# Optimization experiments

Hardware: AMD Instinct MI355X
Metric: run time of the kernel (lower is better)

The kernel has to match this reference:

```python
import jax, jax.numpy as jnp
import numpy as np

N_NODES = 100000
N_EDGES = 1600000
IN_FEATS = 128
N_HIDDEN = 128
N_CLASSES = 47


def setup_inputs() -> dict:
    key = jax.random.key(0)
    ks = jax.random.split(key, 9)
    x = jax.random.normal(ks[0], (N_NODES, IN_FEATS), dtype=jnp.float32)
    src = jax.random.randint(ks[1], (N_EDGES,), 0, N_NODES, dtype=jnp.int32)
    dst = jax.random.randint(ks[2], (N_EDGES,), 0, N_NODES, dtype=jnp.int32)
    s = 0.05
    return {
        "x": x, "src": src, "dst": dst,
        "Ws0": jax.random.normal(ks[3], (IN_FEATS, N_HIDDEN), jnp.float32) * s,
        "Wn0": jax.random.normal(ks[4], (IN_FEATS, N_HIDDEN), jnp.float32) * s,
        "b0": jnp.zeros((N_HIDDEN,), jnp.float32),
        "Ws1": jax.random.normal(ks[5], (N_HIDDEN, N_HIDDEN), jnp.float32) * s,
        "Wn1": jax.random.normal(ks[6], (N_HIDDEN, N_HIDDEN), jnp.float32) * s,
        "b1": jnp.zeros((N_HIDDEN,), jnp.float32),
        "Ws2": jax.random.normal(ks[7], (N_HIDDEN, N_CLASSES), jnp.float32) * s,
        "Wn2": jax.random.normal(ks[8], (N_HIDDEN, N_CLASSES), jnp.float32) * s,
        "b2": jnp.zeros((N_CLASSES,), jnp.float32),
    }


def _sage_layer(h, src, dst, inv_deg, Ws, Wn, b):
    # weighted (w=1) mean aggregation over in-neighbors: sum(h[src]) / in_degree
    msg = h[src]  # [E, d] irregular gather
    neigh = jax.ops.segment_sum(msg, dst, num_segments=N_NODES) * inv_deg[:, None]
    # DGL SAGEConv 'mean': fc_self(h_self) + fc_neigh(h_neigh), bias on self branch
    return h @ Ws + neigh @ Wn + b


def reference(x, src, dst, Ws0, Wn0, b0, Ws1, Wn1, b1, Ws2, Wn2, b2):
    deg = jax.ops.segment_sum(jnp.ones_like(dst, dtype=x.dtype), dst, num_segments=N_NODES)
    inv_deg = 1.0 / jnp.maximum(deg, 1.0)
    h = _sage_layer(x, src, dst, inv_deg, Ws0, Wn0, b0)
    h = jax.nn.relu(h)  # dropout is identity (eval / p=0)
    h = _sage_layer(h, src, dst, inv_deg, Ws1, Wn1, b1)
    h = jax.nn.relu(h)
    h = _sage_layer(h, src, dst, inv_deg, Ws2, Wn2, b2)
    return jax.nn.log_softmax(h, axis=-1)
```

## Files before the change

### kernel.cpp

```cpp
#include <hip/hip_runtime.h>
#include <hip/hip_bf16.h>

#define NN 100000
#define NE 1600000
#define F 128
#define NCLS 47

#define NPB 256
#define BUCKETS 391
#define ABLK 512
#define ACHUNK (NE / ABLK)

typedef __attribute__((ext_vector_type(8))) short short8;
typedef __attribute__((ext_vector_type(8))) unsigned short u16x8;
typedef __attribute__((ext_vector_type(4))) float f32x4;

#define MFMA16(A, B, C) __builtin_amdgcn_mfma_f32_16x16x32_bf16(A, B, C, 0, 0, 0)

__device__ __forceinline__ unsigned short b16(float f) {
    unsigned int u = __builtin_bit_cast(unsigned int, f);
    unsigned int r = u + 0x7FFFu + ((u >> 16) & 1u);
    return (unsigned short)(r >> 16);
}
__device__ __forceinline__ float bflo(unsigned int u) { return __builtin_bit_cast(float, u << 16); }
__device__ __forceinline__ float bfhi(unsigned int u) { return __builtin_bit_cast(float, u & 0xFFFF0000u); }

__global__ void __launch_bounds__(256) k_bhist(const int* __restrict__ dst,
                                               int* __restrict__ bucket_cnt) {
    __shared__ int hist[BUCKETS];
    const int t = threadIdx.x;
    for (int i = t; i < BUCKETS; i += 256) hist[i] = 0;
    __syncthreads();
    const int e0 = blockIdx.x * ACHUNK;
    for (int i = t; i < ACHUNK; i += 256) atomicAdd(&hist[dst[e0 + i] >> 8], 1);
    __syncthreads();
    for (int i = t; i < BUCKETS; i += 256)
        if (hist[i]) atomicAdd(&bucket_cnt[i], hist[i]);
}

__global__ void k_bscan(const int* __restrict__ bucket_cnt, int* __restrict__ bucket_off,
                        int* __restrict__ cursor) {
    const int lane = threadIdx.x & 63;
    int run = 0;
#pragma unroll
    for (int c = 0; c < 7; c++) {
        int idx = c * 64 + lane;
        int v = (idx < BUCKETS) ? bucket_cnt[idx] : 0;
        int s = v;
#pragma unroll
        for (int off = 1; off < 64; off <<= 1) {
            int n = __shfl_up(s, off);
            if (lane >= off) s += n;
        }
        int excl = run + s - v;
        if (idx <= BUCKETS) {
            bucket_off[idx] = excl;
            cursor[idx] = excl;
        }
        run += __shfl(s, 63);
    }
}

__global__ void __launch_bounds__(256) k_bscatter(const int* __restrict__ src,
                                                  const int* __restrict__ dst,
                                                  int* __restrict__ cursor,
                                                  unsigned int* __restrict__ ebuf) {
    __shared__ int hist[BUCKETS];
    __shared__ int base[BUCKETS];
    __shared__ int rank[BUCKETS];
    const int t = threadIdx.x;
    for (int i = t; i < BUCKETS; i += 256) {
        hist[i] = 0;
        rank[i] = 0;
    }
    __syncthreads();
    const int e0 = blockIdx.x * ACHUNK;
    for (int i = t; i < ACHUNK; i += 256) atomicAdd(&hist[dst[e0 + i] >> 8], 1);
    __syncthreads();
    for (int i = t; i < BUCKETS; i += 256) {
        int h = hist[i];
        base[i] = h ? atomicAdd(&cursor[i], h) : 0;
    }
    __syncthreads();
    for (int i = t; i < ACHUNK; i += 256) {
        unsigned int s = (unsigned int)src[e0 + i];
        int d = dst[e0 + i];
        int b = d >> 8;
        int r = atomicAdd(&rank[b], 1);
        ebuf[base[b] + r] = s | ((unsigned int)(d & 255) << 24);
    }
}

__global__ void __launch_bounds__(256) k_bcsr(const unsigned int* __restrict__ ebuf,
                                              const int* __restrict__ bucket_off,
                                              int* __restrict__ row_off,
                                              float* __restrict__ inv_deg,
                                              int* __restrict__ col) {
    __shared__ int cnt[NPB];
    __shared__ int ro[NPB];
    __shared__ int wsum[4];
    const int t = threadIdx.x, lane = t & 63, wid = t >> 6;
    cnt[t] = 0;
    __syncthreads();
    const int e0 = bucket_off[blockIdx.x], e1 = bucket_off[blockIdx.x + 1];
    for (int i = e0 + t; i < e1; i += 256) atomicAdd(&cnt[ebuf[i] >> 24], 1);
    __syncthreads();
    int v = cnt[t];
    int run = v;
#pragma unroll
    for (int off = 1; off < 64; off <<= 1) {
        int n = __shfl_up(run, off);
        if (lane >= off) run += n;
    }
    if (lane == 63) wsum[wid] = run;
    __syncthreads();
    int woff = e0;
#pragma unroll
    for (int wv = 0; wv < 4; wv++)
        if (wv < wid) woff += wsum[wv];
    int excl = woff + run - v;
    int node = (blockIdx.x << 8) + t;
    if (node < NN) {
        row_off[node] = excl;
        inv_deg[node] = 1.0f / fmaxf((float)v, 1.0f);
    }
    if (blockIdx.x == BUCKETS - 1 && t == 0) row_off[NN] = NE;
    ro[t] = excl;
    cnt[t] = 0;
    __syncthreads();
    for (int i = e0 + t; i < e1; i += 256) {
        unsigned int e = ebuf[i];
        int d = e >> 24;
        int p = atomicAdd(&cnt[d], 1);
        col[ro[d] + p] = (int)(e & 0xFFFFFFu);
    }
}

__global__ void k_cvt(const float* __restrict__ x, unsigned short* __restrict__ xb,
                      unsigned short* __restrict__ h1b, unsigned short* __restrict__ hw2b) {
    int t = blockIdx.x * blockDim.x + threadIdx.x;
    if (blockIdx.x == 0) {
        int tt = threadIdx.x;
        if (tt < 128) {
            xb[(size_t)NN * F + tt] = 0;
            h1b[(size_t)NN * F + tt] = 0;
            if (tt < 64) hw2b[(size_t)NN * 64 + tt] = 0;
        }
    }
    if (t >= NN * F / 8) return;
    const float4* x4 = (const float4*)x;
    float4 a = x4[t * 2], b = x4[t * 2 + 1];
    u16x8 o;
    o[0] = b16(a.x); o[1] = b16(a.y); o[2] = b16(a.z); o[3] = b16(a.w);
    o[4] = b16(b.x); o[5] = b16(b.y); o[6] = b16(b.z); o[7] = b16(b.w);
    ((u16x8*)xb)[t] = o;
}

__global__ void k_pack_all(const float* __restrict__ Ws0, const float* __restrict__ Wn0,
                           const float* __restrict__ Ws1, const float* __restrict__ Wn1,
                           const float* __restrict__ Ws2, const float* __restrict__ Wn2,
                           unsigned short* __restrict__ wp) {
    int idx = blockIdx.x * blockDim.x + threadIdx.x;
    if (idx >= 77824) return;
    const float* W;
    int base, ncols;
    if (idx < 65536) {
        int m = idx >> 14;
        W = (m == 0) ? Ws0 : (m == 1) ? Wn0 : (m == 2) ? Ws1 : Wn1;
        base = m << 14;
        ncols = 128;
    } else {
        int m = (idx - 65536) / 6144;
        W = m ? Wn2 : Ws2;
        base = 65536 + m * 6144;
        ncols = NCLS;
    }
    int li = idx - base;
    int nt = li >> 11;
    int r = li & 2047;
    int kk = r >> 9;
    int r2 = r & 511;
    int lane = r2 >> 3;
    int j = r2 & 7;
    int k = kk * 32 + ((lane >> 4) << 3) + j;
    int n = nt * 16 + (lane & 15);
    float v = (n < ncols) ? W[k * ncols + n] : 0.f;
    wp[idx] = b16(v);
}

__global__ void __launch_bounds__(256) k_aggb(const uint4* __restrict__ h4,
                                              const int* __restrict__ row_off,
                                              const int* __restrict__ col,
                                              const float* __restrict__ inv_deg,
                                              uint4* __restrict__ a4) {
    int node = (blockIdx.x * blockDim.x + threadIdx.x) >> 6;
    int lane = threadIdx.x & 63;
    if (node >= NN) return;
    int b = row_off[node], e = row_off[node + 1];
    int deg = e - b;
    const int g = lane >> 4, fl = lane & 15;
    float acc[8];
#pragma unroll
    for (int i = 0; i < 8; i++) acc[i] = 0.f;
    for (int base = 0; base < deg; base += 64) {
        int cnt = deg - base;
        if (cnt > 64) cnt = 64;
        int myc = col[b + base + (lane < cnt ? lane : 0)];
        for (int jj = 0; jj < cnt; jj += 16) {
            uint4 u[4];
#pragma unroll
            for (int k2 = 0; k2 < 4; k2++) {
                int r = jj + k2 * 4 + g;
                int c = __shfl(myc, r);
                c = (r < cnt) ? c : NN;
                u[k2] = h4[(size_t)(unsigned)c * 16u + fl];
            }
#pragma unroll
            for (int k2 = 0; k2 < 4; k2++) {
                uint4 v = u[k2];
                acc[0] += bflo(v.x); acc[1] += bfhi(v.x);
                acc[2] += bflo(v.y); acc[3] += bfhi(v.y);
                acc[4] += bflo(v.z); acc[5] += bfhi(v.z);
                acc[6] += bflo(v.w); acc[7] += bfhi(v.w);
            }
        }
    }
#pragma unroll
    for (int i = 0; i < 8; i++) {
        acc[i] += __shfl_xor(acc[i], 16);
        acc[i] += __shfl_xor(acc[i], 32);
    }
    if (g == 0) {
        float s = inv_deg[node];
        uint4 o;
        o.x = (unsigned)b16(acc[0] * s) | ((unsigned)b16(acc[1] * s) << 16);
        o.y = (unsigned)b16(acc[2] * s) | ((unsigned)b16(acc[3] * s) << 16);
        o.z = (unsigned)b16(acc[4] * s) | ((unsigned)b16(acc[5] * s) << 16);
        o.w = (unsigned)b16(acc[6] * s) | ((unsigned)b16(acc[7] * s) << 16);
        a4[(size_t)node * 16 + fl] = o;
    }
}

__global__ void __launch_bounds__(256) k_agg48(const uint4* __restrict__ hw4,
                                               const int* __restrict__ row_off,
                                               const int* __restrict__ col,
                                               const float* __restrict__ inv_deg,
                                               uint4* __restrict__ aggh4) {
    int node = (blockIdx.x * blockDim.x + threadIdx.x) >> 6;
    int lane = threadIdx.x & 63;
    if (node >= NN) return;
    int b = row_off[node], e = row_off[node + 1];
    int deg = e - b;
    const int g = lane >> 3, fl = lane & 7;
    float acc[8];
#pragma unroll
    for (int i = 0; i < 8; i++) acc[i] = 0.f;
    for (int base = 0; base < deg; base += 64) {
        int cnt = deg - base;
        if (cnt > 64) cnt = 64;
        int myc = col[b + base + (lane < cnt ? lane : 0)];
        for (int jj = 0; jj < cnt; jj += 16) {
            uint4 u[2];
#pragma unroll
            for (int k2 = 0; k2 < 2; k2++) {
                int r = jj + k2 * 8 + g;
                int c = __shfl(myc, r);
                c = (r < cnt) ? c : NN;
                u[k2] = hw4[(size_t)(unsigned)c * 8u + fl];
            }
#pragma unroll
            for (int k2 = 0; k2 < 2; k2++) {
                uint4 v = u[k2];
                acc[0] += bflo(v.x); acc[1] += bfhi(v.x);
                acc[2] += bflo(v.y); acc[3] += bfhi(v.y);
                acc[4] += bflo(v.z); acc[5] += bfhi(v.z);
                acc[6] += bflo(v.w); acc[7] += bfhi(v.w);
            }
        }
    }
#pragma unroll
    for (int i = 0; i < 8; i++) {
        acc[i] += __shfl_xor(acc[i], 8);
        acc[i] += __shfl_xor(acc[i], 16);
        acc[i] += __shfl_xor(acc[i], 32);
    }
    if (lane < 8) {
        float s = inv_deg[node];
        uint4 o;
        o.x = (unsigned)b16(acc[0] * s) | ((unsigned)b16(acc[1] * s) << 16);
        o.y = (unsigned)b16(acc[2] * s) | ((unsigned)b16(acc[3] * s) << 16);
        o.z = (unsigned)b16(acc[4] * s) | ((unsigned)b16(acc[5] * s) << 16);
        o.w = (unsigned)b16(acc[6] * s) | ((unsigned)b16(acc[7] * s) << 16);
        aggh4[(size_t)node * 8 + fl] = o;
    }
}

template <bool RELU>
__global__ void __launch_bounds__(256) k_layer(const unsigned short* __restrict__ hb,
                                               const unsigned short* __restrict__ ab,
                                               const unsigned short* __restrict__ wps,
                                               const unsigned short* __restrict__ wpn,
                                               const float* __restrict__ bias,
                                               unsigned short* __restrict__ outb) {
    const int wid = threadIdx.x >> 6, lane = threadIdx.x & 63;
    const int tile0 = blockIdx.x * 64;
    const short8* ws8 = (const short8*)wps;
    const short8* wn8 = (const short8*)wpn;
    short8 wf[2][2][4];
#pragma unroll
    for (int t = 0; t < 2; t++) {
        int nt = 2 * wid + t;
#pragma unroll
        for (int kk = 0; kk < 4; kk++) {
            wf[0][t][kk] = ws8[(nt * 4 + kk) * 64 + lane];
            wf[1][t][kk] = wn8[(nt * 4 + kk) * 64 + lane];
        }
    }
    const int rb = lane & 15, kq = lane >> 4;
    float bv[2];
#pragma unroll
    for (int t = 0; t < 2; t++) bv[t] = bias[(2 * wid + t) * 16 + rb];
    const short8* h8 = (const short8*)hb;
    const short8* a8 = (const short8*)ab;
    f32x4 zero = {0.f, 0.f, 0.f, 0.f};
    f32x4 acc[4][2];
#pragma unroll
    for (int m = 0; m < 4; m++)
#pragma unroll
        for (int t = 0; t < 2; t++) acc[m][t] = zero;
#pragma unroll
    for (int kk = 0; kk < 4; kk++) {
#pragma unroll
        for (int m = 0; m < 4; m++) {
            int row = tile0 + m * 16 + rb;
            int rc = row < NN ? row : NN - 1;
            int idx = rc * 16 + kk * 4 + kq;
            short8 af = h8[idx];
            short8 gf = a8[idx];
            acc[m][0] = MFMA16(af, wf[0][0][kk], acc[m][0]);
            acc[m][1] = MFMA16(af, wf[0][1][kk], acc[m][1]);
            acc[m][0] = MFMA16(gf, wf[1][0][kk], acc[m][0]);
            acc[m][1] = MFMA16(gf, wf[1][1][kk], acc[m][1]);
        }
    }
#pragma unroll
    for (int m = 0; m < 4; m++) {
#pragma unroll
        for (int reg = 0; reg < 4; reg++) {
            int row = tile0 + m * 16 + kq * 4 + reg;
            if (row < NN) {
#pragma unroll
                for (int t = 0; t < 2; t++) {
                    float v = acc[m][t][reg] + bv[t];
                    if (RELU) v = fmaxf(v, 0.f);
                    outb[(size_t)row * F + (2 * wid + t) * 16 + rb] = b16(v);
                }
            }
        }
    }
}

__global__ void __launch_bounds__(512) k_nmul(const unsigned short* __restrict__ hb,
                                              const unsigned short* __restrict__ wpn,
                                              unsigned short* __restrict__ hw) {
    const int wid = threadIdx.x >> 6, lane = threadIdx.x & 63;
    const int R0 = blockIdx.x * 128 + wid * 16;
    const short8* wn8 = (const short8*)wpn;
    short8 wf[3][4];
#pragma unroll
    for (int nt = 0; nt < 3; nt++)
#pragma unroll
        for (int kk = 0; kk < 4; kk++) wf[nt][kk] = wn8[(nt * 4 + kk) * 64 + lane];
    const int rb = lane & 15, kq = lane >> 4;
    const short8* h8 = (const short8*)hb;
    f32x4 zero = {0.f, 0.f, 0.f, 0.f};
    f32x4 acc[3] = {zero, zero, zero};
    int rowr = R0 + rb;
    int rc = rowr < NN ? rowr : NN - 1;
#pragma unroll
    for (int kk = 0; kk < 4; kk++) {
        short8 af = h8[rc * 16 + kk * 4 + kq];
#pragma unroll
        for (int nt = 0; nt < 3; nt++) acc[nt] = MFMA16(af, wf[nt][kk], acc[nt]);
    }
#pragma unroll
    for (int reg = 0; reg < 4; reg++) {
        int row = R0 + kq * 4 + reg;
        if (row < NN) {
#pragma unroll
            for (int nt = 0; nt < 3; nt++)
                hw[(size_t)row * 64 + nt * 16 + rb] = b16(acc[nt][reg]);
        }
    }
}

__global__ void __launch_bounds__(512) k_out2(const unsigned short* __restrict__ hb,
                                              const unsigned short* __restrict__ aggh,
                                              const unsigned short* __restrict__ wps,
                                              const float* __restrict__ bias,
                                              float* __restrict__ out) {
    const int wid = threadIdx.x >> 6, lane = threadIdx.x & 63;
    const int R0 = blockIdx.x * 128 + wid * 16;
    const short8* ws8 = (const short8*)wps;
    short8 wf[3][4];
#pragma unroll
    for (int nt = 0; nt < 3; nt++)
#pragma unroll
        for (int kk = 0; kk < 4; kk++) wf[nt][kk] = ws8[(nt * 4 + kk) * 64 + lane];
    const int rb = lane & 15, kq = lane >> 4;
    float bv[3];
    bool valid[3];
#pragma unroll
    for (int nt = 0; nt < 3; nt++) {
        int c = nt * 16 + rb;
        valid[nt] = c < NCLS;
        bv[nt] = valid[nt] ? bias[c] : 0.f;
    }
    const short8* h8 = (const short8*)hb;
    f32x4 zero = {0.f, 0.f, 0.f, 0.f};
    f32x4 acc[3] = {zero, zero, zero};
    int rowr = R0 + rb;
    int rc = rowr < NN ? rowr : NN - 1;
#pragma unroll
    for (int kk = 0; kk < 4; kk++) {
        short8 af = h8[rc * 16 + kk * 4 + kq];
#pragma unroll
        for (int nt = 0; nt < 3; nt++) acc[nt] = MFMA16(af, wf[nt][kk], acc[nt]);
    }
#pragma unroll
    for (int reg = 0; reg < 4; reg++) {
        int row = R0 + kq * 4 + reg;
        int rc2 = row < NN ? row : NN - 1;
        float v[3];
        float mx = -1e30f;
#pragma unroll
        for (int nt = 0; nt < 3; nt++) {
            float av = __builtin_bit_cast(
                float, (unsigned)aggh[(size_t)rc2 * 64 + nt * 16 + rb] << 16);
            v[nt] = acc[nt][reg] + av + bv[nt];
            if (valid[nt]) mx = fmaxf(mx, v[nt]);
        }
        for (int off = 1; off < 16; off <<= 1) mx = fmaxf(mx, __shfl_xor(mx, off));
        float s = 0.f;
#pragma unroll
        for (int nt = 0; nt < 3; nt++)
            if (valid[nt]) s += expf(v[nt] - mx);
        for (int off = 1; off < 16; off <<= 1) s += __shfl_xor(s, off);
        float L = mx + logf(s);
        if (row < NN) {
#pragma unroll
            for (int nt = 0; nt < 3; nt++)
                if (valid[nt]) out[(size_t)row * NCLS + nt * 16 + rb] = v[nt] - L;
        }
    }
}

extern "C" void kernel_launch(void* const* d_in, const int* in_sizes, int n_in,
                              void* d_out, int out_size, void* d_ws, size_t ws_size,
                              hipStream_t stream) {
    (void)in_sizes; (void)n_in; (void)out_size; (void)ws_size;
    const float* x = (const float*)d_in[0];
    const int* src = (const int*)d_in[1];
    const int* dst = (const int*)d_in[2];
    const float* Ws0 = (const float*)d_in[3];
    const float* Wn0 = (const float*)d_in[4];
    const float* b0 = (const float*)d_in[5];
    const float* Ws1 = (const float*)d_in[6];
    const float* Wn1 = (const float*)d_in[7];
    const float* b1 = (const float*)d_in[8];
    const float* Ws2 = (const float*)d_in[9];
    const float* Wn2 = (const float*)d_in[10];
    const float* b2 = (const float*)d_in[11];
    float* out = (float*)d_out;

    char* w = (char*)d_ws;
    size_t off = 0;
    auto alloc = [&](size_t bytes) -> char* {
        char* p = w + off;
        off = (off + bytes + 255) & ~(size_t)255;
        return p;
    };
    int* row_off = (int*)alloc((size_t)(NN + 1) * 4);
    int* col = (int*)alloc((size_t)NE * 4);
    float* inv_deg = (float*)alloc((size_t)NN * 4);
    int* bucket_cnt = (int*)alloc((size_t)(BUCKETS + 1) * 4);
    int* bucket_off = (int*)alloc((size_t)(BUCKETS + 1) * 4);
    int* bcursor = (int*)alloc((size_t)(BUCKETS + 1) * 4);
    unsigned int* ebuf = (unsigned int*)alloc((size_t)(NN + 1) * 64 * 2);
    unsigned short* xb = (unsigned short*)alloc((size_t)(NN + 1) * F * 2);
    unsigned short* aggb = (unsigned short*)alloc((size_t)NN * F * 2);
    unsigned short* h1b = (unsigned short*)alloc((size_t)(NN + 1) * F * 2);
    unsigned short* h2b = (unsigned short*)alloc((size_t)NN * F * 2);
    unsigned short* wp = (unsigned short*)alloc((size_t)77824 * 2);

    unsigned short* hw2b = (unsigned short*)ebuf;
    unsigned short* aggh = aggb;

    hipMemsetAsync(bucket_cnt, 0, (size_t)(BUCKETS + 1) * 4, stream);

    k_bhist<<<ABLK, 256, 0, stream>>>(dst, bucket_cnt);
    k_bscan<<<1, 64, 0, stream>>>(bucket_cnt, bucket_off, bcursor);
    k_bscatter<<<ABLK, 256, 0, stream>>>(src, dst, bcursor, ebuf);
    k_bcsr<<<BUCKETS, 256, 0, stream>>>(ebuf, bucket_off, row_off, inv_deg, col);

    k_cvt<<<(NN * F / 8 + 255) / 256, 256, 0, stream>>>(x, xb, h1b, hw2b);
    k_pack_all<<<(77824 + 255) / 256, 256, 0, stream>>>(Ws0, Wn0, Ws1, Wn1, Ws2, Wn2, wp);

    unsigned short* wS0 = wp;
    unsigned short* wN0 = wp + 16384;
    unsigned short* wS1 = wp + 32768;
    unsigned short* wN1 = wp + 49152;
    unsigned short* wS2 = wp + 65536;
    unsigned short* wN2 = wp + 71680;

    const int AGG_B = NN * 64 / 256;
    const int LYR_B = (NN + 63) / 64;
    const int OUT_B = (NN + 127) / 128;

    k_aggb<<<AGG_B, 256, 0, stream>>>((const uint4*)xb, row_off, col, inv_deg, (uint4*)aggb);
    k_layer<true><<<LYR_B, 256, 0, stream>>>(xb, aggb, wS0, wN0, b0, h1b);
    k_aggb<<<AGG_B, 256, 0, stream>>>((const uint4*)h1b, row_off, col, inv_deg, (uint4*)aggb);
    k_layer<true><<<LYR_B, 256, 0, stream>>>(h1b, aggb, wS1, wN1, b1, h2b);
    k_nmul<<<OUT_B, 512, 0, stream>>>(h2b, wN2, hw2b);
    k_agg48<<<AGG_B, 256, 0, stream>>>((const uint4*)hw2b, row_off, col, inv_deg,
                                       (uint4*)aggh);
    k_out2<<<OUT_B, 512, 0, stream>>>(h2b, aggh, wS2, b2, out);
}
```

Before: 321.8 us.

## Use fixed-capacity dst buckets and fuse final neighbor matmul into layer kernel

```diff
diff --git a/kernel.cpp b/kernel.cpp
--- a/kernel.cpp
+++ b/kernel.cpp
@@ -8,6 +8,7 @@
 
 #define NPB 256
 #define BUCKETS 391
+#define CAP 4608
 #define ABLK 512
 #define ACHUNK (NE / ABLK)
 
@@ -25,45 +26,9 @@
 __device__ __forceinline__ float bflo(unsigned int u) { return __builtin_bit_cast(float, u << 16); }
 __device__ __forceinline__ float bfhi(unsigned int u) { return __builtin_bit_cast(float, u & 0xFFFF0000u); }
 
-__global__ void __launch_bounds__(256) k_bhist(const int* __restrict__ dst,
-                                               int* __restrict__ bucket_cnt) {
-    __shared__ int hist[BUCKETS];
-    const int t = threadIdx.x;
-    for (int i = t; i < BUCKETS; i += 256) hist[i] = 0;
-    __syncthreads();
-    const int e0 = blockIdx.x * ACHUNK;
-    for (int i = t; i < ACHUNK; i += 256) atomicAdd(&hist[dst[e0 + i] >> 8], 1);
-    __syncthreads();
-    for (int i = t; i < BUCKETS; i += 256)
-        if (hist[i]) atomicAdd(&bucket_cnt[i], hist[i]);
-}
-
-__global__ void k_bscan(const int* __restrict__ bucket_cnt, int* __restrict__ bucket_off,
-                        int* __restrict__ cursor) {
-    const int lane = threadIdx.x & 63;
-    int run = 0;
-#pragma unroll
-    for (int c = 0; c < 7; c++) {
-        int idx = c * 64 + lane;
-        int v = (idx < BUCKETS) ? bucket_cnt[idx] : 0;
-        int s = v;
-#pragma unroll
-        for (int off = 1; off < 64; off <<= 1) {
-            int n = __shfl_up(s, off);
-            if (lane >= off) s += n;
-        }
-        int excl = run + s - v;
-        if (idx <= BUCKETS) {
-            bucket_off[idx] = excl;
-            cursor[idx] = excl;
-        }
-        run += __shfl(s, 63);
-    }
-}
-
 __global__ void __launch_bounds__(256) k_bscatter(const int* __restrict__ src,
                                                   const int* __restrict__ dst,
-                                                  int* __restrict__ cursor,
+                                                  int* __restrict__ bucket_cnt,
                                                   unsigned int* __restrict__ ebuf) {
     __shared__ int hist[BUCKETS];
     __shared__ int base[BUCKETS];
@@ -79,7 +44,7 @@
     __syncthreads();
     for (int i = t; i < BUCKETS; i += 256) {
         int h = hist[i];
-        base[i] = h ? atomicAdd(&cursor[i], h) : 0;
+        base[i] = h ? atomicAdd(&bucket_cnt[i], h) : 0;
     }
     __syncthreads();
     for (int i = t; i < ACHUNK; i += 256) {
@@ -87,13 +52,13 @@
         int d = dst[e0 + i];
         int b = d >> 8;
         int r = atomicAdd(&rank[b], 1);
-        ebuf[base[b] + r] = s | ((unsigned int)(d & 255) << 24);
+        ebuf[(size_t)b * CAP + base[b] + r] = s | ((unsigned int)(d & 255) << 24);
     }
 }
 
 __global__ void __launch_bounds__(256) k_bcsr(const unsigned int* __restrict__ ebuf,
-                                              const int* __restrict__ bucket_off,
-                                              int* __restrict__ row_off,
+                                              const int* __restrict__ bucket_cnt,
+                                              int2* __restrict__ nfo,
                                               float* __restrict__ inv_deg,
                                               int* __restrict__ col) {
     __shared__ int cnt[NPB];
@@ -102,7 +67,8 @@
     const int t = threadIdx.x, lane = t & 63, wid = t >> 6;
     cnt[t] = 0;
     __syncthreads();
-    const int e0 = bucket_off[blockIdx.x], e1 = bucket_off[blockIdx.x + 1];
+    const int e0 = blockIdx.x * CAP;
+    const int e1 = e0 + bucket_cnt[blockIdx.x];
     for (int i = e0 + t; i < e1; i += 256) atomicAdd(&cnt[ebuf[i] >> 24], 1);
     __syncthreads();
     int v = cnt[t];
@@ -121,10 +87,9 @@
     int excl = woff + run - v;
     int node = (blockIdx.x << 8) + t;
     if (node < NN) {
-        row_off[node] = excl;
+        nfo[node] = make_int2(excl, v);
         inv_deg[node] = 1.0f / fmaxf((float)v, 1.0f);
     }
-    if (blockIdx.x == BUCKETS - 1 && t == 0) row_off[NN] = NE;
     ro[t] = excl;
     cnt[t] = 0;
     __syncthreads();
@@ -189,15 +154,15 @@
 }
 
 __global__ void __launch_bounds__(256) k_aggb(const uint4* __restrict__ h4,
-                                              const int* __restrict__ row_off,
+                                              const int2* __restrict__ nfo,
                                               const int* __restrict__ col,
                                               const float* __restrict__ inv_deg,
                                               uint4* __restrict__ a4) {
     int node = (blockIdx.x * blockDim.x + threadIdx.x) >> 6;
     int lane = threadIdx.x & 63;
     if (node >= NN) return;
-    int b = row_off[node], e = row_off[node + 1];
-    int deg = e - b;
+    int2 f = nfo[node];
+    int b = f.x, deg = f.y;
     const int g = lane >> 4, fl = lane & 15;
     float acc[8];
 #pragma unroll
@@ -242,15 +207,15 @@
 }
 
 __global__ void __launch_bounds__(256) k_agg48(const uint4* __restrict__ hw4,
-                                               const int* __restrict__ row_off,
+                                               const int2* __restrict__ nfo,
                                                const int* __restrict__ col,
                                                const float* __restrict__ inv_deg,
                                                uint4* __restrict__ aggh4) {
     int node = (blockIdx.x * blockDim.x + threadIdx.x) >> 6;
     int lane = threadIdx.x & 63;
     if (node >= NN) return;
-    int b = row_off[node], e = row_off[node + 1];
-    int deg = e - b;
+    int2 f = nfo[node];
+    int b = f.x, deg = f.y;
     const int g = lane >> 3, fl = lane & 7;
     float acc[8];
 #pragma unroll
@@ -295,13 +260,16 @@
     }
 }
 
-template <bool RELU>
+template <bool RELU, bool NMUL>
 __global__ void __launch_bounds__(256) k_layer(const unsigned short* __restrict__ hb,
                                                const unsigned short* __restrict__ ab,
                                                const unsigned short* __restrict__ wps,
                                                const unsigned short* __restrict__ wpn,
                                                const float* __restrict__ bias,
-                                               unsigned short* __restrict__ outb) {
+                                               unsigned short* __restrict__ outb,
+                                               const unsigned short* __restrict__ wpn2,
+                                               unsigned short* __restrict__ hw) {
+    __shared__ unsigned short tile[NMUL ? 64 * 136 : 1];
     const int wid = threadIdx.x >> 6, lane = threadIdx.x & 63;
     const int tile0 = blockIdx.x * 64;
     const short8* ws8 = (const short8*)wps;
@@ -348,48 +316,40 @@
 #pragma unroll
         for (int reg = 0; reg < 4; reg++) {
             int row = tile0 + m * 16 + kq * 4 + reg;
+#pragma unroll
+            for (int t = 0; t < 2; t++) {
+                float v = acc[m][t][reg] + bv[t];
+                if (RELU) v = fmaxf(v, 0.f);
+                unsigned short us = b16(v);
+                if (row < NN) outb[(size_t)row * F + (2 * wid + t) * 16 + rb] = us;
+                if (NMUL) tile[(m * 16 + kq * 4 + reg) * 136 + (2 * wid + t) * 16 + rb] = us;
+            }
+        }
+    }
+    if (NMUL) {
+        __syncthreads();
+        const short8* wn28 = (const short8*)wpn2;
+        short8 wf2[3][4];
+#pragma unroll
+        for (int nt = 0; nt < 3; nt++)
+#pragma unroll
+            for (int kk = 0; kk < 4; kk++) wf2[nt][kk] = wn28[(nt * 4 + kk) * 64 + lane];
+        f32x4 acc2[3] = {zero, zero, zero};
+        const int rloc = wid * 16 + rb;
+#pragma unroll
+        for (int kk = 0; kk < 4; kk++) {
+            short8 af = *(const short8*)&tile[rloc * 136 + kk * 32 + kq * 8];
+#pragma unroll
+            for (int nt = 0; nt < 3; nt++) acc2[nt] = MFMA16(af, wf2[nt][kk], acc2[nt]);
+        }
+#pragma unroll
+        for (int reg = 0; reg < 4; reg++) {
+            int row = tile0 + wid * 16 + kq * 4 + reg;
             if (row < NN) {
 #pragma unroll
-                for (int t = 0; t < 2; t++) {
-                    float v = acc[m][t][reg] + bv[t];
-                    if (RELU) v = fmaxf(v, 0.f);
-                    outb[(size_t)row * F + (2 * wid + t) * 16 + rb] = b16(v);
-                }
-            }
-        }
-    }
-}
-
-__global__ void __launch_bounds__(512) k_nmul(const unsigned short* __restrict__ hb,
-                                              const unsigned short* __restrict__ wpn,
-                                              unsigned short* __restrict__ hw) {
-    const int wid = threadIdx.x >> 6, lane = threadIdx.x & 63;
-    const int R0 = blockIdx.x * 128 + wid * 16;
-    const short8* wn8 = (const short8*)wpn;
-    short8 wf[3][4];
-#pragma unroll
-    for (int nt = 0; nt < 3; nt++)
-#pragma unroll
-        for (int kk = 0; kk < 4; kk++) wf[nt][kk] = wn8[(nt * 4 + kk) * 64 + lane];
-    const int rb = lane & 15, kq = lane >> 4;
-    const short8* h8 = (const short8*)hb;
-    f32x4 zero = {0.f, 0.f, 0.f, 0.f};
-    f32x4 acc[3] = {zero, zero, zero};
-    int rowr = R0 + rb;
-    int rc = rowr < NN ? rowr : NN - 1;
-#pragma unroll
-    for (int kk = 0; kk < 4; kk++) {
-        short8 af = h8[rc * 16 + kk * 4 + kq];
-#pragma unroll
-        for (int nt = 0; nt < 3; nt++) acc[nt] = MFMA16(af, wf[nt][kk], acc[nt]);
-    }
-#pragma unroll
-    for (int reg = 0; reg < 4; reg++) {
-        int row = R0 + kq * 4 + reg;
-        if (row < NN) {
-#pragma unroll
-            for (int nt = 0; nt < 3; nt++)
-                hw[(size_t)row * 64 + nt * 16 + rb] = b16(acc[nt][reg]);
+                for (int nt = 0; nt < 3; nt++)
+                    hw[(size_t)row * 64 + nt * 16 + rb] = b16(acc2[nt][reg]);
+            }
         }
     }
 }
@@ -480,12 +440,10 @@
         off = (off + bytes + 255) & ~(size_t)255;
         return p;
     };
-    int* row_off = (int*)alloc((size_t)(NN + 1) * 4);
-    int* col = (int*)alloc((size_t)NE * 4);
+    int2* nfo = (int2*)alloc((size_t)NN * 8);
+    int* col = (int*)alloc((size_t)BUCKETS * CAP * 4);
     float* inv_deg = (float*)alloc((size_t)NN * 4);
     int* bucket_cnt = (int*)alloc((size_t)(BUCKETS + 1) * 4);
-    int* bucket_off = (int*)alloc((size_t)(BUCKETS + 1) * 4);
-    int* bcursor = (int*)alloc((size_t)(BUCKETS + 1) * 4);
     unsigned int* ebuf = (unsigned int*)alloc((size_t)(NN + 1) * 64 * 2);
     unsigned short* xb = (unsigned short*)alloc((size_t)(NN + 1) * F * 2);
     unsigned short* aggb = (unsigned short*)alloc((size_t)NN * F * 2);
@@ -498,10 +456,8 @@
 
     hipMemsetAsync(bucket_cnt, 0, (size_t)(BUCKETS + 1) * 4, stream);
 
-    k_bhist<<<ABLK, 256, 0, stream>>>(dst, bucket_cnt);
-    k_bscan<<<1, 64, 0, stream>>>(bucket_cnt, bucket_off, bcursor);
-    k_bscatter<<<ABLK, 256, 0, stream>>>(src, dst, bcursor, ebuf);
-    k_bcsr<<<BUCKETS, 256, 0, stream>>>(ebuf, bucket_off, row_off, inv_deg, col);
+    k_bscatter<<<ABLK, 256, 0, stream>>>(src, dst, bucket_cnt, ebuf);
+    k_bcsr<<<BUCKETS, 256, 0, stream>>>(ebuf, bucket_cnt, nfo, inv_deg, col);
 
     k_cvt<<<(NN * F / 8 + 255) / 256, 256, 0, stream>>>(x, xb, h1b, hw2b);
     k_pack_all<<<(77824 + 255) / 256, 256, 0, stream>>>(Ws0, Wn0, Ws1, Wn1, Ws2, Wn2, wp);
@@ -517,12 +473,11 @@
     const int LYR_B = (NN + 63) / 64;
     const int OUT_B = (NN + 127) / 128;
 
-    k_aggb<<<AGG_B, 256, 0, stream>>>((const uint4*)xb, row_off, col, inv_deg, (uint4*)aggb);
-    k_layer<true><<<LYR_B, 256, 0, stream>>>(xb, aggb, wS0, wN0, b0, h1b);
-    k_aggb<<<AGG_B, 256, 0, stream>>>((const uint4*)h1b, row_off, col, inv_deg, (uint4*)aggb);
-    k_layer<true><<<LYR_B, 256, 0, stream>>>(h1b, aggb, wS1, wN1, b1, h2b);
-    k_nmul<<<OUT_B, 512, 0, stream>>>(h2b, wN2, hw2b);
-    k_agg48<<<AGG_B, 256, 0, stream>>>((const uint4*)hw2b, row_off, col, inv_deg,
-                                       (uint4*)aggh);
+    k_aggb<<<AGG_B, 256, 0, stream>>>((const uint4*)xb, nfo, col, inv_deg, (uint4*)aggb);
+    k_layer<true, false><<<LYR_B, 256, 0, stream>>>(xb, aggb, wS0, wN0, b0, h1b, nullptr,
+                                                    nullptr);
+    k_aggb<<<AGG_B, 256, 0, stream>>>((const uint4*)h1b, nfo, col, inv_deg, (uint4*)aggb);
+    k_layer<true, true><<<LYR_B, 256, 0, stream>>>(h1b, aggb, wS1, wN1, b1, h2b, wN2, hw2b);
+    k_agg48<<<AGG_B, 256, 0, stream>>>((const uint4*)hw2b, nfo, col, inv_deg, (uint4*)aggh);
     k_out2<<<OUT_B, 512, 0, stream>>>(h2b, aggh, wS2, b2, out);
 }
```

Measured after the change: 298.9 us, median of 2. -7.1%, faster.
